# Performance work log

Measured on AMD Instinct MI355X. Metric: run time of the kernel, lower is better.

## Reference

```python
import jax, jax.numpy as jnp
import numpy as np

N = 200000   # active voxel sites
G = 80       # voxel grid extent per axis
K = 27       # 3x3x3 kernel offsets
CIN = 64
COUT = 128
EPS = 1e-5


def _build_rulebook(seed=0):
    """Submanifold 3x3x3 rulebook: for each offset k and output site i,
    in_idx[k,i] = index of neighbor site (or 0 if absent),
    out_idx[k,i] = i (or N = dummy row if neighbor absent)."""
    rng = np.random.default_rng(seed)
    lin = rng.choice(G ** 3, size=N, replace=False).astype(np.int64)
    lut = np.full(G ** 3, -1, dtype=np.int64)
    lut[lin] = np.arange(N)
    cx, cy, cz = lin // (G * G), (lin // G) % G, lin % G
    offs = [(dx, dy, dz) for dx in (-1, 0, 1) for dy in (-1, 0, 1) for dz in (-1, 0, 1)]
    in_idx = np.zeros((K, N), np.int32)
    out_idx = np.full((K, N), N, np.int32)
    ar = np.arange(N, dtype=np.int32)
    for k, (dx, dy, dz) in enumerate(offs):
        nx, ny, nz = cx + dx, cy + dy, cz + dz
        ok = (nx >= 0) & (nx < G) & (ny >= 0) & (ny < G) & (nz >= 0) & (nz < G)
        nb_lin = np.where(ok, nx * G * G + ny * G + nz, 0)
        j = lut[nb_lin]
        valid = ok & (j >= 0)
        in_idx[k] = np.where(valid, j, 0).astype(np.int32)
        out_idx[k] = np.where(valid, ar, N)
    return jnp.asarray(in_idx), jnp.asarray(out_idx)


def setup_inputs() -> dict:
    key = jax.random.key(0)
    ks = jax.random.split(key, 8)
    in_idx, out_idx = _build_rulebook(0)
    s1 = 1.0 / np.sqrt(CIN * K)
    s2 = 1.0 / np.sqrt(COUT * K)
    ss = 1.0 / np.sqrt(CIN)
    return {
        "feats": jax.random.normal(ks[0], (N, CIN), jnp.float32),
        "in_idx": in_idx,
        "out_idx": out_idx,
        "W1": jax.random.normal(ks[1], (K, CIN, COUT), jnp.float32) * s1,
        "g1": jnp.ones((COUT,), jnp.float32) + 0.1 * jax.random.normal(ks[2], (COUT,), jnp.float32),
        "b1": 0.1 * jax.random.normal(ks[3], (COUT,), jnp.float32),
        "W2": jax.random.normal(ks[4], (K, COUT, COUT), jnp.float32) * s2,
        "g2": jnp.ones((COUT,), jnp.float32) + 0.1 * jax.random.normal(ks[5], (COUT,), jnp.float32),
        "b2": 0.1 * jax.random.normal(ks[6], (COUT,), jnp.float32),
        "Wsc": jax.random.normal(ks[7], (CIN, COUT), jnp.float32) * ss,
        "gsc": jnp.ones((COUT,), jnp.float32),
        "bsc": jnp.zeros((COUT,), jnp.float32),
    }


def _spconv(feats, W, in_idx, out_idx):
    """Rulebook gather-GEMM-scatter sparse conv. feats [N,Cin], W [K,Cin,Cout]."""
    cout = W.shape[-1]
    out = jnp.zeros((N + 1, cout), feats.dtype)  # row N = dummy for padded pairs
    for k in range(K):  # fixed small structural loop over kernel offsets
        out = out.at[out_idx[k]].add(feats[in_idx[k]] @ W[k])
    return out[:N]


def _bn(x, gamma, beta):
    # training-mode BatchNorm over the site dimension (biased variance)
    m = jnp.mean(x, axis=0)
    v = jnp.var(x, axis=0)
    return (x - m) * jax.lax.rsqrt(v + EPS) * gamma + beta


def reference(feats, in_idx, out_idx, W1, g1, b1, W2, g2, b2, Wsc, gsc, bsc):
    h = jax.nn.relu(_bn(_spconv(feats, W1, in_idx, out_idx), g1, b1))
    h = _bn(_spconv(h, W2, in_idx, out_idx), g2, b2)
    sc = _bn(feats @ Wsc, gsc, bsc)  # 1x1 sparse conv == per-site linear
    return jax.nn.relu(h + sc)
```

## Files before the change

kernel.cpp:

```cpp
#include <hip/hip_runtime.h>

#define NS 200000
#define NK 27
#define NB2 1563
#define EPSV 1e-5f

typedef __bf16 bf16x8 __attribute__((ext_vector_type(8)));
typedef float f32x4 __attribute__((ext_vector_type(4)));
typedef unsigned short u16;
typedef u16 u16x8 __attribute__((ext_vector_type(8)));
typedef u16 u16x4 __attribute__((ext_vector_type(4)));
typedef unsigned u32;

__device__ __forceinline__ u16 f2bf(float f) {
  union { float f; unsigned u; } v; v.f = f;
  unsigned r = v.u + 0x7fffu + ((v.u >> 16) & 1u);
  return (u16)(r >> 16);
}
__device__ __forceinline__ float bf2f(u16 u) {
  union { unsigned u; float f; } v; v.u = ((unsigned)u) << 16;
  return v.f;
}

__global__ void k_prep_x(const float* __restrict__ feats, u16* __restrict__ Xbf,
                         float* __restrict__ stats) {
  long i = (long)blockIdx.x * 256 + threadIdx.x;
  if (i < 768) stats[i] = 0.f;
  const long total = (long)(NS + 1) * 64;
  if (i < total) {
    long row = i >> 6;
    Xbf[i] = (row < NS) ? f2bf(feats[i]) : (u16)0;
  }
}

__global__ void k_prep_gidx(const int* __restrict__ in_idx, const int* __restrict__ out_idx,
                            int* __restrict__ gidx) {
  long i = (long)blockIdx.x * 256 + threadIdx.x;
  if (i < (long)NK * NS) gidx[i] = (out_idx[i] != NS) ? in_idx[i] : NS;
}

__global__ void k_pack_w(const float* __restrict__ W1, const float* __restrict__ W2,
                         const float* __restrict__ Wsc, u16* __restrict__ Wp1,
                         u16* __restrict__ Wp2, u16* __restrict__ Wpsc) {
  int i = blockIdx.x * 256 + threadIdx.x;
  const int n1 = NK * 64 * 128, n2 = NK * 128 * 128, n3 = 64 * 128;
  const float* src; u16* dst; int f, S, C;
  if (i < n1)            { src = W1;  dst = Wp1;  f = i;            S = 2; C = 64; }
  else if (i < n1 + n2)  { src = W2;  dst = Wp2;  f = i - n1;       S = 4; C = 128; }
  else if (i < n1 + n2 + n3) { src = Wsc; dst = Wpsc; f = i - n1 - n2; S = 2; C = 64; }
  else return;
  int j = f & 7, q = (f >> 3) & 3, r = (f >> 5) & 15, cf = (f >> 9) & 7;
  int rest = f >> 12;
  int s = rest % S, k = rest / S;
  int kk = s * 32 + q * 8 + j;
  dst[f] = f2bf(src[(k * C + kk) * 128 + cf * 16 + r]);
}

template <int C, bool FUSE_SC>
__global__ __launch_bounds__(256, (C == 64) ? 3 : 2) void k_conv(
    const u16* __restrict__ X, const u16* __restrict__ Wp, const u16* __restrict__ Wpsc,
    const int* __restrict__ gidx,
    u16* __restrict__ Y, u16* __restrict__ SCb, float* __restrict__ partial) {
  constexpr int S = C / 32;
  constexpr int SLICE = C * 128;
  constexpr int NST = SLICE / 2048;
  constexpr int NG = 2 * S;
  constexpr int NW_STEADY = NG + 2 + NST + NG + 2;
  constexpr int PC = FUSE_SC ? 512 : 256;
  __shared__ alignas(16) u16 Wbuf[2 * SLICE];
  float* red = reinterpret_cast<float*>(&Wbuf[2 * SLICE - 2048]);

  const int t = threadIdx.x, w = t >> 6, l = t & 63;
  const int lr = l & 15, lh = l >> 4;
  const int rowbase = blockIdx.x * 128 + w * 32;
  const int laneoff = lr * 32 + lh * 8;

  int rr[2]; bool ok[2]; long rc[2];
  #pragma unroll
  for (int m = 0; m < 2; ++m) {
    rr[m] = rowbase + m * 16 + lr;
    ok[m] = rr[m] < NS;
    rc[m] = ok[m] ? rr[m] : 0;
  }

  auto stage = [&](int k, int bsel) {
    #pragma unroll
    for (int i = 0; i < NST; ++i) {
      const u16* g = Wp + (long)k * SLICE + (w * NST + i) * 512 + l * 8;
      u16* d = &Wbuf[bsel * SLICE + (w * NST + i) * 512];
      __builtin_amdgcn_global_load_lds(
          (const __attribute__((address_space(1))) u32*)g,
          (__attribute__((address_space(3))) u32*)d, 16, 0, 0);
    }
  };
  auto loadidx = [&](int k, int (&dst)[2]) {
    #pragma unroll
    for (int m = 0; m < 2; ++m) {
      int v = gidx[(long)k * NS + rc[m]];
      dst[m] = ok[m] ? v : NS;
    }
  };
  auto gather = [&](const int (&src)[2], bf16x8 (&a)[2][S]) {
    #pragma unroll
    for (int m = 0; m < 2; ++m) {
      const u16* rowp = X + (long)src[m] * C + lh * 8;
      #pragma unroll
      for (int s = 0; s < S; ++s)
        a[m][s] = *reinterpret_cast<const bf16x8*>(rowp + s * 32);
    }
  };
  auto compute = [&](int bsel, const bf16x8 (&a)[2][S], f32x4 (&ac)[2][8]) {
    #pragma unroll
    for (int s = 0; s < S; ++s)
      #pragma unroll
      for (int cf = 0; cf < 8; ++cf) {
        bf16x8 b = *reinterpret_cast<const bf16x8*>(&Wbuf[bsel * SLICE + (s * 8 + cf) * 512 + laneoff]);
        ac[0][cf] = __builtin_amdgcn_mfma_f32_16x16x32_bf16(a[0][s], b, ac[0][cf], 0, 0, 0);
        ac[1][cf] = __builtin_amdgcn_mfma_f32_16x16x32_bf16(a[1][s], b, ac[1][cf], 0, 0, 0);
      }
  };
  auto emit = [&](f32x4 (&ac)[2][8], u16* __restrict__ Yp, int poff) {
    #pragma unroll
    for (int m = 0; m < 2; ++m)
      #pragma unroll
      for (int cf = 0; cf < 8; ++cf) {
        int ch = cf * 16 + lr;
        #pragma unroll
        for (int r = 0; r < 4; ++r) {
          long row = rowbase + m * 16 + lh * 4 + r;
          if (row < NS) Yp[row * 128 + ch] = f2bf(ac[m][cf][r]);
        }
      }
    __syncthreads();
    #pragma unroll
    for (int cf = 0; cf < 8; ++cf) {
      float s = 0.f, q = 0.f;
      #pragma unroll
      for (int m = 0; m < 2; ++m)
        #pragma unroll
        for (int r = 0; r < 4; ++r) { float v = ac[m][cf][r]; s += v; q += v * v; }
      s += __shfl_xor(s, 16); s += __shfl_xor(s, 32);
      q += __shfl_xor(q, 16); q += __shfl_xor(q, 32);
      if (lh == 0) {
        red[w * 256 + cf * 16 + lr] = s;
        red[w * 256 + 128 + cf * 16 + lr] = q;
      }
    }
    __syncthreads();
    if (t < 256)
      partial[(long)blockIdx.x * PC + poff + t] =
          red[t] + red[256 + t] + red[512 + t] + red[768 + t];
    __syncthreads();
  };

  int sv0[2], sv1[2];
  bf16x8 av0[2][S], av1[2][S];
  loadidx(0, sv0);
  stage(0, 0);
  gather(sv0, av0);
  loadidx(1, sv1);

  if constexpr (FUSE_SC) {
    bf16x8 ai[2][S];
    #pragma unroll
    for (int m = 0; m < 2; ++m) {
      long srcr = ok[m] ? rr[m] : NS;
      #pragma unroll
      for (int s = 0; s < S; ++s)
        ai[m][s] = *reinterpret_cast<const bf16x8*>(X + srcr * C + lh * 8 + s * 32);
    }
    f32x4 asc[2][8];
    #pragma unroll
    for (int m = 0; m < 2; ++m)
      #pragma unroll
      for (int cf = 0; cf < 8; ++cf) asc[m][cf] = (f32x4){0.f, 0.f, 0.f, 0.f};
    #pragma unroll
    for (int s = 0; s < S; ++s)
      #pragma unroll
      for (int cf = 0; cf < 8; ++cf) {
        bf16x8 b = *reinterpret_cast<const bf16x8*>(Wpsc + (s * 8 + cf) * 512 + laneoff);
        asc[0][cf] = __builtin_amdgcn_mfma_f32_16x16x32_bf16(ai[0][s], b, asc[0][cf], 0, 0, 0);
        asc[1][cf] = __builtin_amdgcn_mfma_f32_16x16x32_bf16(ai[1][s], b, asc[1][cf], 0, 0, 0);
      }
    emit(asc, SCb, 256);
  }

  f32x4 acc[2][8];
  #pragma unroll
  for (int m = 0; m < 2; ++m)
    #pragma unroll
    for (int cf = 0; cf < 8; ++cf) acc[m][cf] = (f32x4){0.f, 0.f, 0.f, 0.f};

  #pragma unroll 1
  for (int k = 0; k < 24; k += 2) {
    stage(k + 1, 1);
    gather(sv1, av1);
    loadidx(k + 2, sv0);
    asm volatile("s_waitcnt vmcnt(%0)\n\ts_barrier" :: "i"(NW_STEADY) : "memory");
    compute(0, av0, acc);
    asm volatile("s_waitcnt lgkmcnt(0)\n\ts_barrier" ::: "memory");

    stage(k + 2, 0);
    gather(sv0, av0);
    loadidx(k + 3, sv1);
    asm volatile("s_waitcnt vmcnt(%0)\n\ts_barrier" :: "i"(NW_STEADY) : "memory");
    compute(1, av1, acc);
    asm volatile("s_waitcnt lgkmcnt(0)\n\ts_barrier" ::: "memory");
  }
  stage(25, 1);
  gather(sv1, av1);
  loadidx(26, sv0);
  asm volatile("s_waitcnt vmcnt(%0)\n\ts_barrier" :: "i"(NW_STEADY) : "memory");
  compute(0, av0, acc);
  asm volatile("s_waitcnt lgkmcnt(0)\n\ts_barrier" ::: "memory");

  stage(26, 0);
  gather(sv0, av0);
  asm volatile("s_waitcnt vmcnt(%0)\n\ts_barrier" :: "i"(NW_STEADY - 2) : "memory");
  compute(1, av1, acc);
  asm volatile("s_waitcnt lgkmcnt(0)\n\ts_barrier" ::: "memory");

  asm volatile("s_waitcnt vmcnt(%0)\n\ts_barrier" :: "i"(NG) : "memory");
  compute(0, av0, acc);

  emit(acc, Y, 0);
}

__global__ void k_red1(const float* __restrict__ part, float* __restrict__ tmp,
                       int pc, int nrows) {
  int c = blockIdx.x * 256 + threadIdx.x;
  float s = 0.f;
  for (int r = blockIdx.y; r < nrows; r += 32) s += part[(long)r * pc + c];
  tmp[(long)blockIdx.y * pc + c] = s;
}
__global__ void k_red2(const float* __restrict__ tmp, float* __restrict__ out, int pc) {
  int c = blockIdx.x * 256 + threadIdx.x;
  float s = 0.f;
  #pragma unroll
  for (int r = 0; r < 32; ++r) s += tmp[(long)r * pc + c];
  out[c] = s;
}

__global__ void k_bnrelu(const u16* __restrict__ Y1, const float* __restrict__ stats,
                         const float* __restrict__ g, const float* __restrict__ b,
                         u16* __restrict__ H) {
  long i8 = (long)blockIdx.x * 256 + threadIdx.x;
  const long tot = (long)(NS + 1) * 16;
  if (i8 >= tot) return;
  long row = i8 >> 4;
  u16x8 o;
  if (row < NS) {
    int ch0 = ((int)i8 & 15) * 8;
    u16x8 y = *reinterpret_cast<const u16x8*>(Y1 + i8 * 8);
    #pragma unroll
    for (int e = 0; e < 8; ++e) {
      int ch = ch0 + e;
      float m = stats[ch] * (1.f / NS);
      float var = stats[128 + ch] * (1.f / NS) - m * m;
      float a = g[ch] * rsqrtf(var + EPSV);
      float bb = b[ch] - m * a;
      float h = bf2f(y[e]) * a + bb;
      o[e] = f2bf(h > 0.f ? h : 0.f);
    }
  } else {
    #pragma unroll
    for (int e = 0; e < 8; ++e) o[e] = (u16)0;
  }
  *reinterpret_cast<u16x8*>(H + i8 * 8) = o;
}

__global__ void k_final(const u16* __restrict__ Y2, const u16* __restrict__ SCb,
                        const float* __restrict__ stats,
                        const float* __restrict__ g2, const float* __restrict__ b2,
                        const float* __restrict__ gsc, const float* __restrict__ bsc,
                        float* __restrict__ out) {
  long i4 = (long)blockIdx.x * 256 + threadIdx.x;
  if (i4 >= (long)NS * 32) return;
  int ch0 = ((int)i4 & 31) * 4;
  u16x4 y = *reinterpret_cast<const u16x4*>(Y2 + i4 * 4);
  u16x4 s = *reinterpret_cast<const u16x4*>(SCb + i4 * 4);
  f32x4 o;
  #pragma unroll
  for (int e = 0; e < 4; ++e) {
    int ch = ch0 + e;
    float m2 = stats[512 + ch] * (1.f / NS);
    float v2 = stats[640 + ch] * (1.f / NS) - m2 * m2;
    float a2 = g2[ch] * rsqrtf(v2 + EPSV);
    float msc = stats[256 + ch] * (1.f / NS);
    float vsc = stats[384 + ch] * (1.f / NS) - msc * msc;
    float asc = gsc[ch] * rsqrtf(vsc + EPSV);
    float val = bf2f(y[e]) * a2 + (b2[ch] - m2 * a2)
              + bf2f(s[e]) * asc + (bsc[ch] - msc * asc);
    o[e] = val > 0.f ? val : 0.f;
  }
  *reinterpret_cast<f32x4*>(out + i4 * 4) = o;
}

extern "C" void kernel_launch(void* const* d_in, const int* in_sizes, int n_in,
                              void* d_out, int out_size, void* d_ws, size_t ws_size,
                              hipStream_t stream) {
  const float* feats = (const float*)d_in[0];
  const int* in_idx  = (const int*)d_in[1];
  const int* out_idx = (const int*)d_in[2];
  const float* W1  = (const float*)d_in[3];
  const float* g1  = (const float*)d_in[4];
  const float* b1  = (const float*)d_in[5];
  const float* W2  = (const float*)d_in[6];
  const float* g2  = (const float*)d_in[7];
  const float* b2  = (const float*)d_in[8];
  const float* Wsc = (const float*)d_in[9];
  const float* gsc = (const float*)d_in[10];
  const float* bsc = (const float*)d_in[11];

  char* ws = (char*)d_ws;
  size_t off = 0;
  auto alloc = [&](size_t bytes) {
    void* p = ws + off; off += (bytes + 255) & ~(size_t)255; return p;
  };
  float* stats = (float*)alloc(768 * 4);
  float* rtmp  = (float*)alloc(32 * 512 * 4);
  u16* Xbf  = (u16*)alloc((size_t)(NS + 1) * 64 * 2);
  u16* SCbf = (u16*)alloc((size_t)NS * 128 * 2);
  u16* Hbf  = (u16*)alloc((size_t)(NS + 1) * 128 * 2);
  u16* Y2bf = (u16*)alloc((size_t)NS * 128 * 2);
  u16* Wp1  = (u16*)alloc((size_t)NK * 64 * 128 * 2);
  u16* Wp2  = (u16*)alloc((size_t)NK * 128 * 128 * 2);
  u16* Wpsc = (u16*)alloc((size_t)64 * 128 * 2);
  u16* Y1bf = (u16*)d_out;
  int* gidx = (int*)((char*)d_out + (size_t)NS * 128 * 2);
  float* part1 = (float*)Y2bf;
  float* part2 = (float*)Xbf;

  hipLaunchKernelGGL(k_prep_x, dim3(50001), dim3(256), 0, stream, feats, Xbf, stats);
  hipLaunchKernelGGL(k_prep_gidx, dim3((NK * NS + 255) / 256), dim3(256), 0, stream,
                     in_idx, out_idx, gidx);
  hipLaunchKernelGGL(k_pack_w, dim3(2624), dim3(256), 0, stream, W1, W2, Wsc, Wp1, Wp2, Wpsc);
  hipLaunchKernelGGL((k_conv<64, true>), dim3(NB2), dim3(256), 0, stream,
                     Xbf, Wp1, Wpsc, gidx, Y1bf, SCbf, part1);
  hipLaunchKernelGGL(k_red1, dim3(2, 32), dim3(256), 0, stream, part1, rtmp, 512, NB2);
  hipLaunchKernelGGL(k_red2, dim3(2), dim3(256), 0, stream, rtmp, stats, 512);
  hipLaunchKernelGGL(k_bnrelu, dim3(12501), dim3(256), 0, stream, Y1bf, stats, g1, b1, Hbf);
  hipLaunchKernelGGL((k_conv<128, false>), dim3(NB2), dim3(256), 0, stream,
                     Hbf, Wp2, nullptr, gidx, Y2bf, nullptr, part2);
  hipLaunchKernelGGL(k_red1, dim3(1, 32), dim3(256), 0, stream, part2, rtmp, 256, NB2);
  hipLaunchKernelGGL(k_red2, dim3(1), dim3(256), 0, stream, rtmp, stats + 512, 256);
  hipLaunchKernelGGL(k_final, dim3(25000), dim3(256), 0, stream,
                     Y2bf, SCbf, stats, g2, b2, gsc, bsc, (float*)d_out);
}
```

Before: 480.9 us.

## Double conv block size to 512 threads and repack weights for linear LDS reads

The sparse conv kernel now runs 8 waves per block covering 256 rows, so each staged weight slice in LDS is shared by twice as many rows and the grid is halved. The packed weight layout changes so each lane reads a contiguous 16-byte chunk (laneoff = l*8), which aims to cut LDS bank conflicts. The reduction buffer moves to its own shared array, one barrier is dropped, and MFMA sections are raised in wave priority with s_setprio. The larger block and separate reduction buffer raise LDS and register pressure per block, which may lower occupancy.

```diff
diff --git a/kernel.cpp b/kernel.cpp
--- a/kernel.cpp
+++ b/kernel.cpp
@@ -2,7 +2,7 @@
 
 #define NS 200000
 #define NK 27
-#define NB2 1563
+#define NBLK 782
 #define EPSV 1e-5f
 
 typedef __bf16 bf16x8 __attribute__((ext_vector_type(8)));
@@ -49,31 +49,31 @@
   else if (i < n1 + n2)  { src = W2;  dst = Wp2;  f = i - n1;       S = 4; C = 128; }
   else if (i < n1 + n2 + n3) { src = Wsc; dst = Wpsc; f = i - n1 - n2; S = 2; C = 64; }
   else return;
-  int j = f & 7, q = (f >> 3) & 3, r = (f >> 5) & 15, cf = (f >> 9) & 7;
+  int j = f & 7, l = (f >> 3) & 63, cf = (f >> 9) & 7;
   int rest = f >> 12;
   int s = rest % S, k = rest / S;
-  int kk = s * 32 + q * 8 + j;
-  dst[f] = f2bf(src[(k * C + kk) * 128 + cf * 16 + r]);
+  int kk = s * 32 + (l >> 4) * 8 + j;
+  dst[f] = f2bf(src[(k * C + kk) * 128 + cf * 16 + (l & 15)]);
 }
 
 template <int C, bool FUSE_SC>
-__global__ __launch_bounds__(256, (C == 64) ? 3 : 2) void k_conv(
+__global__ __launch_bounds__(512, 4) void k_conv(
     const u16* __restrict__ X, const u16* __restrict__ Wp, const u16* __restrict__ Wpsc,
     const int* __restrict__ gidx,
     u16* __restrict__ Y, u16* __restrict__ SCb, float* __restrict__ partial) {
   constexpr int S = C / 32;
   constexpr int SLICE = C * 128;
-  constexpr int NST = SLICE / 2048;
+  constexpr int NST = SLICE / 4096;
   constexpr int NG = 2 * S;
   constexpr int NW_STEADY = NG + 2 + NST + NG + 2;
   constexpr int PC = FUSE_SC ? 512 : 256;
   __shared__ alignas(16) u16 Wbuf[2 * SLICE];
-  float* red = reinterpret_cast<float*>(&Wbuf[2 * SLICE - 2048]);
+  __shared__ float red[2048];
 
   const int t = threadIdx.x, w = t >> 6, l = t & 63;
   const int lr = l & 15, lh = l >> 4;
-  const int rowbase = blockIdx.x * 128 + w * 32;
-  const int laneoff = lr * 32 + lh * 8;
+  const int rowbase = blockIdx.x * 256 + w * 32;
+  const int laneoff = l * 8;
 
   int rr[2]; bool ok[2]; long rc[2];
   #pragma unroll
@@ -110,6 +110,7 @@
     }
   };
   auto compute = [&](int bsel, const bf16x8 (&a)[2][S], f32x4 (&ac)[2][8]) {
+    __builtin_amdgcn_s_setprio(1);
     #pragma unroll
     for (int s = 0; s < S; ++s)
       #pragma unroll
@@ -118,6 +119,7 @@
         ac[0][cf] = __builtin_amdgcn_mfma_f32_16x16x32_bf16(a[0][s], b, ac[0][cf], 0, 0, 0);
         ac[1][cf] = __builtin_amdgcn_mfma_f32_16x16x32_bf16(a[1][s], b, ac[1][cf], 0, 0, 0);
       }
+    __builtin_amdgcn_s_setprio(0);
   };
   auto emit = [&](f32x4 (&ac)[2][8], u16* __restrict__ Yp, int poff) {
     #pragma unroll
@@ -131,7 +133,6 @@
           if (row < NS) Yp[row * 128 + ch] = f2bf(ac[m][cf][r]);
         }
       }
-    __syncthreads();
     #pragma unroll
     for (int cf = 0; cf < 8; ++cf) {
       float s = 0.f, q = 0.f;
@@ -147,9 +148,12 @@
       }
     }
     __syncthreads();
-    if (t < 256)
-      partial[(long)blockIdx.x * PC + poff + t] =
-          red[t] + red[256 + t] + red[512 + t] + red[768 + t];
+    if (t < 256) {
+      float sum = 0.f;
+      #pragma unroll
+      for (int wi = 0; wi < 8; ++wi) sum += red[wi * 256 + t];
+      partial[(long)blockIdx.x * PC + poff + t] = sum;
+    }
     __syncthreads();
   };
 
@@ -335,14 +339,14 @@
   hipLaunchKernelGGL(k_prep_gidx, dim3((NK * NS + 255) / 256), dim3(256), 0, stream,
                      in_idx, out_idx, gidx);
   hipLaunchKernelGGL(k_pack_w, dim3(2624), dim3(256), 0, stream, W1, W2, Wsc, Wp1, Wp2, Wpsc);
-  hipLaunchKernelGGL((k_conv<64, true>), dim3(NB2), dim3(256), 0, stream,
+  hipLaunchKernelGGL((k_conv<64, true>), dim3(NBLK), dim3(512), 0, stream,
                      Xbf, Wp1, Wpsc, gidx, Y1bf, SCbf, part1);
-  hipLaunchKernelGGL(k_red1, dim3(2, 32), dim3(256), 0, stream, part1, rtmp, 512, NB2);
+  hipLaunchKernelGGL(k_red1, dim3(2, 32), dim3(256), 0, stream, part1, rtmp, 512, NBLK);
   hipLaunchKernelGGL(k_red2, dim3(2), dim3(256), 0, stream, rtmp, stats, 512);
   hipLaunchKernelGGL(k_bnrelu, dim3(12501), dim3(256), 0, stream, Y1bf, stats, g1, b1, Hbf);
-  hipLaunchKernelGGL((k_conv<128, false>), dim3(NB2), dim3(256), 0, stream,
+  hipLaunchKernelGGL((k_conv<128, false>), dim3(NBLK), dim3(512), 0, stream,
                      Hbf, Wp2, nullptr, gidx, Y2bf, nullptr, part2);
-  hipLaunchKernelGGL(k_red1, dim3(1, 32), dim3(256), 0, stream, part2, rtmp, 256, NB2);
+  hipLaunchKernelGGL(k_red1, dim3(1, 32), dim3(256), 0, stream, part2, rtmp, 256, NBLK);
   hipLaunchKernelGGL(k_red2, dim3(1), dim3(256), 0, stream, rtmp, stats + 512, 256);
   hipLaunchKernelGGL(k_final, dim3(25000), dim3(256), 0, stream,
                      Y2bf, SCbf, stats, g2, b2, gsc, bsc, (float*)d_out);
```

Result: slower. 707.3 us (+47.1%).

## Skip gathers for absent neighbors, restructure conv pipeline waits, add MFMA priority

Applied to the files above, without the earlier changes.

The conv main loop is restructured. Each gather is issued after a barrier that waits only on staged weights and index loads, and the epilogue is folded into the loop by clamping the last index load. Gathers for missing neighbors are now skipped and zero-filled, so the padded dummy row and its write in prep and bnrelu are removed. Compute sections raise wave priority with s_setprio, and the weight packing and LDS read offset change to a linear per-lane layout. The aim is less wasted memory traffic on sparse neighbors and better overlap, at the cost of gathers now sitting closer to the compute that uses them.

```diff
diff --git a/kernel.cpp b/kernel.cpp
--- a/kernel.cpp
+++ b/kernel.cpp
@@ -2,7 +2,7 @@
 
 #define NS 200000
 #define NK 27
-#define NB2 1563
+#define NB 1563
 #define EPSV 1e-5f
 
 typedef __bf16 bf16x8 __attribute__((ext_vector_type(8)));
@@ -26,11 +26,8 @@
                          float* __restrict__ stats) {
   long i = (long)blockIdx.x * 256 + threadIdx.x;
   if (i < 768) stats[i] = 0.f;
-  const long total = (long)(NS + 1) * 64;
-  if (i < total) {
-    long row = i >> 6;
-    Xbf[i] = (row < NS) ? f2bf(feats[i]) : (u16)0;
-  }
+  const long total = (long)NS * 64;
+  if (i < total) Xbf[i] = f2bf(feats[i]);
 }
 
 __global__ void k_prep_gidx(const int* __restrict__ in_idx, const int* __restrict__ out_idx,
@@ -49,11 +46,11 @@
   else if (i < n1 + n2)  { src = W2;  dst = Wp2;  f = i - n1;       S = 4; C = 128; }
   else if (i < n1 + n2 + n3) { src = Wsc; dst = Wpsc; f = i - n1 - n2; S = 2; C = 64; }
   else return;
-  int j = f & 7, q = (f >> 3) & 3, r = (f >> 5) & 15, cf = (f >> 9) & 7;
+  int j = f & 7, l = (f >> 3) & 63, cf = (f >> 9) & 7;
   int rest = f >> 12;
   int s = rest % S, k = rest / S;
-  int kk = s * 32 + q * 8 + j;
-  dst[f] = f2bf(src[(k * C + kk) * 128 + cf * 16 + r]);
+  int kk = s * 32 + (l >> 4) * 8 + j;
+  dst[f] = f2bf(src[(k * C + kk) * 128 + cf * 16 + (l & 15)]);
 }
 
 template <int C, bool FUSE_SC>
@@ -63,17 +60,16 @@
     u16* __restrict__ Y, u16* __restrict__ SCb, float* __restrict__ partial) {
   constexpr int S = C / 32;
   constexpr int SLICE = C * 128;
-  constexpr int NST = SLICE / 2048;
-  constexpr int NG = 2 * S;
-  constexpr int NW_STEADY = NG + 2 + NST + NG + 2;
+  constexpr int NST = C / 16;
+  constexpr int WAITN = NST + 4;
   constexpr int PC = FUSE_SC ? 512 : 256;
   __shared__ alignas(16) u16 Wbuf[2 * SLICE];
-  float* red = reinterpret_cast<float*>(&Wbuf[2 * SLICE - 2048]);
+  float* red = reinterpret_cast<float*>(Wbuf);
 
   const int t = threadIdx.x, w = t >> 6, l = t & 63;
   const int lr = l & 15, lh = l >> 4;
   const int rowbase = blockIdx.x * 128 + w * 32;
-  const int laneoff = lr * 32 + lh * 8;
+  const int laneoff = l * 8;
 
   int rr[2]; bool ok[2]; long rc[2];
   #pragma unroll
@@ -83,11 +79,11 @@
     rc[m] = ok[m] ? rr[m] : 0;
   }
 
-  auto stage = [&](int k, int bsel) {
+  auto stage = [&](int k, int p) {
     #pragma unroll
     for (int i = 0; i < NST; ++i) {
       const u16* g = Wp + (long)k * SLICE + (w * NST + i) * 512 + l * 8;
-      u16* d = &Wbuf[bsel * SLICE + (w * NST + i) * 512];
+      u16* d = &Wbuf[p * SLICE + (w * NST + i) * 512];
       __builtin_amdgcn_global_load_lds(
           (const __attribute__((address_space(1))) u32*)g,
           (__attribute__((address_space(3))) u32*)d, 16, 0, 0);
@@ -103,21 +99,28 @@
   auto gather = [&](const int (&src)[2], bf16x8 (&a)[2][S]) {
     #pragma unroll
     for (int m = 0; m < 2; ++m) {
-      const u16* rowp = X + (long)src[m] * C + lh * 8;
-      #pragma unroll
-      for (int s = 0; s < S; ++s)
-        a[m][s] = *reinterpret_cast<const bf16x8*>(rowp + s * 32);
-    }
-  };
-  auto compute = [&](int bsel, const bf16x8 (&a)[2][S], f32x4 (&ac)[2][8]) {
+      #pragma unroll
+      for (int s = 0; s < S; ++s) a[m][s] = bf16x8{};
+      if (src[m] != NS) {
+        const u16* rowp = X + (long)src[m] * C + lh * 8;
+        #pragma unroll
+        for (int s = 0; s < S; ++s)
+          a[m][s] = *reinterpret_cast<const bf16x8*>(rowp + s * 32);
+      }
+    }
+  };
+  auto compute = [&](int p, const bf16x8 (&a)[2][S], f32x4 (&ac)[2][8]) {
+    __builtin_amdgcn_s_setprio(1);
     #pragma unroll
     for (int s = 0; s < S; ++s)
       #pragma unroll
       for (int cf = 0; cf < 8; ++cf) {
-        bf16x8 b = *reinterpret_cast<const bf16x8*>(&Wbuf[bsel * SLICE + (s * 8 + cf) * 512 + laneoff]);
+        bf16x8 b = *reinterpret_cast<const bf16x8*>(
+            &Wbuf[p * SLICE + (s * 8 + cf) * 512 + laneoff]);
         ac[0][cf] = __builtin_amdgcn_mfma_f32_16x16x32_bf16(a[0][s], b, ac[0][cf], 0, 0, 0);
         ac[1][cf] = __builtin_amdgcn_mfma_f32_16x16x32_bf16(a[1][s], b, ac[1][cf], 0, 0, 0);
       }
+    __builtin_amdgcn_s_setprio(0);
   };
   auto emit = [&](f32x4 (&ac)[2][8], u16* __restrict__ Yp, int poff) {
     #pragma unroll
@@ -153,74 +156,64 @@
     __syncthreads();
   };
 
+  if constexpr (FUSE_SC) {
+    bf16x8 ai[2][2];
+    #pragma unroll
+    for (int m = 0; m < 2; ++m) {
+      #pragma unroll
+      for (int s = 0; s < 2; ++s) ai[m][s] = bf16x8{};
+      if (ok[m]) {
+        #pragma unroll
+        for (int s = 0; s < 2; ++s)
+          ai[m][s] = *reinterpret_cast<const bf16x8*>(X + (long)rr[m] * 64 + lh * 8 + s * 32);
+      }
+    }
+    f32x4 asc[2][8];
+    #pragma unroll
+    for (int m = 0; m < 2; ++m)
+      #pragma unroll
+      for (int cf = 0; cf < 8; ++cf) asc[m][cf] = (f32x4){0.f, 0.f, 0.f, 0.f};
+    #pragma unroll
+    for (int s = 0; s < 2; ++s)
+      #pragma unroll
+      for (int cf = 0; cf < 8; ++cf) {
+        bf16x8 b = *reinterpret_cast<const bf16x8*>(Wpsc + (s * 8 + cf) * 512 + laneoff);
+        asc[0][cf] = __builtin_amdgcn_mfma_f32_16x16x32_bf16(ai[0][s], b, asc[0][cf], 0, 0, 0);
+        asc[1][cf] = __builtin_amdgcn_mfma_f32_16x16x32_bf16(ai[1][s], b, asc[1][cf], 0, 0, 0);
+      }
+    emit(asc, SCb, 256);
+  }
+
+  f32x4 acc[2][8];
+  #pragma unroll
+  for (int m = 0; m < 2; ++m)
+    #pragma unroll
+    for (int cf = 0; cf < 8; ++cf) acc[m][cf] = (f32x4){0.f, 0.f, 0.f, 0.f};
+
   int sv0[2], sv1[2];
   bf16x8 av0[2][S], av1[2][S];
+
   loadidx(0, sv0);
   stage(0, 0);
   gather(sv0, av0);
   loadidx(1, sv1);
 
-  if constexpr (FUSE_SC) {
-    bf16x8 ai[2][S];
-    #pragma unroll
-    for (int m = 0; m < 2; ++m) {
-      long srcr = ok[m] ? rr[m] : NS;
-      #pragma unroll
-      for (int s = 0; s < S; ++s)
-        ai[m][s] = *reinterpret_cast<const bf16x8*>(X + srcr * C + lh * 8 + s * 32);
-    }
-    f32x4 asc[2][8];
-    #pragma unroll
-    for (int m = 0; m < 2; ++m)
-      #pragma unroll
-      for (int cf = 0; cf < 8; ++cf) asc[m][cf] = (f32x4){0.f, 0.f, 0.f, 0.f};
-    #pragma unroll
-    for (int s = 0; s < S; ++s)
-      #pragma unroll
-      for (int cf = 0; cf < 8; ++cf) {
-        bf16x8 b = *reinterpret_cast<const bf16x8*>(Wpsc + (s * 8 + cf) * 512 + laneoff);
-        asc[0][cf] = __builtin_amdgcn_mfma_f32_16x16x32_bf16(ai[0][s], b, asc[0][cf], 0, 0, 0);
-        asc[1][cf] = __builtin_amdgcn_mfma_f32_16x16x32_bf16(ai[1][s], b, asc[1][cf], 0, 0, 0);
-      }
-    emit(asc, SCb, 256);
-  }
-
-  f32x4 acc[2][8];
-  #pragma unroll
-  for (int m = 0; m < 2; ++m)
-    #pragma unroll
-    for (int cf = 0; cf < 8; ++cf) acc[m][cf] = (f32x4){0.f, 0.f, 0.f, 0.f};
-
   #pragma unroll 1
-  for (int k = 0; k < 24; k += 2) {
+  for (int k = 0; k < NK - 1; k += 2) {
     stage(k + 1, 1);
+    loadidx(k + 2, sv0);
+    asm volatile("s_waitcnt vmcnt(%0)\n\ts_barrier" :: "i"(WAITN) : "memory");
     gather(sv1, av1);
-    loadidx(k + 2, sv0);
-    asm volatile("s_waitcnt vmcnt(%0)\n\ts_barrier" :: "i"(NW_STEADY) : "memory");
     compute(0, av0, acc);
     asm volatile("s_waitcnt lgkmcnt(0)\n\ts_barrier" ::: "memory");
-
     stage(k + 2, 0);
+    { int kn = k + 3 < NK ? k + 3 : NK - 1; loadidx(kn, sv1); }
+    asm volatile("s_waitcnt vmcnt(%0)\n\ts_barrier" :: "i"(WAITN) : "memory");
     gather(sv0, av0);
-    loadidx(k + 3, sv1);
-    asm volatile("s_waitcnt vmcnt(%0)\n\ts_barrier" :: "i"(NW_STEADY) : "memory");
     compute(1, av1, acc);
     asm volatile("s_waitcnt lgkmcnt(0)\n\ts_barrier" ::: "memory");
   }
-  stage(25, 1);
-  gather(sv1, av1);
-  loadidx(26, sv0);
-  asm volatile("s_waitcnt vmcnt(%0)\n\ts_barrier" :: "i"(NW_STEADY) : "memory");
-  compute(0, av0, acc);
-  asm volatile("s_waitcnt lgkmcnt(0)\n\ts_barrier" ::: "memory");
-
-  stage(26, 0);
-  gather(sv0, av0);
-  asm volatile("s_waitcnt vmcnt(%0)\n\ts_barrier" :: "i"(NW_STEADY - 2) : "memory");
-  compute(1, av1, acc);
-  asm volatile("s_waitcnt lgkmcnt(0)\n\ts_barrier" ::: "memory");
-
-  asm volatile("s_waitcnt vmcnt(%0)\n\ts_barrier" :: "i"(NG) : "memory");
+  asm volatile("s_waitcnt vmcnt(0)\n\ts_barrier" ::: "memory");
   compute(0, av0, acc);
 
   emit(acc, Y, 0);
@@ -245,26 +238,20 @@
                          const float* __restrict__ g, const float* __restrict__ b,
                          u16* __restrict__ H) {
   long i8 = (long)blockIdx.x * 256 + threadIdx.x;
-  const long tot = (long)(NS + 1) * 16;
+  const long tot = (long)NS * 16;
   if (i8 >= tot) return;
-  long row = i8 >> 4;
+  int ch0 = ((int)i8 & 15) * 8;
+  u16x8 y = *reinterpret_cast<const u16x8*>(Y1 + i8 * 8);
   u16x8 o;
-  if (row < NS) {
-    int ch0 = ((int)i8 & 15) * 8;
-    u16x8 y = *reinterpret_cast<const u16x8*>(Y1 + i8 * 8);
-    #pragma unroll
-    for (int e = 0; e < 8; ++e) {
-      int ch = ch0 + e;
-      float m = stats[ch] * (1.f / NS);
-      float var = stats[128 + ch] * (1.f / NS) - m * m;
-      float a = g[ch] * rsqrtf(var + EPSV);
-      float bb = b[ch] - m * a;
-      float h = bf2f(y[e]) * a + bb;
-      o[e] = f2bf(h > 0.f ? h : 0.f);
-    }
-  } else {
-    #pragma unroll
-    for (int e = 0; e < 8; ++e) o[e] = (u16)0;
+  #pragma unroll
+  for (int e = 0; e < 8; ++e) {
+    int ch = ch0 + e;
+    float m = stats[ch] * (1.f / NS);
+    float var = stats[128 + ch] * (1.f / NS) - m * m;
+    float a = g[ch] * rsqrtf(var + EPSV);
+    float bb = b[ch] - m * a;
+    float h = bf2f(y[e]) * a + bb;
+    o[e] = f2bf(h > 0.f ? h : 0.f);
   }
   *reinterpret_cast<u16x8*>(H + i8 * 8) = o;
 }
@@ -319,9 +306,9 @@
   };
   float* stats = (float*)alloc(768 * 4);
   float* rtmp  = (float*)alloc(32 * 512 * 4);
-  u16* Xbf  = (u16*)alloc((size_t)(NS + 1) * 64 * 2);
+  u16* Xbf  = (u16*)alloc((size_t)NS * 64 * 2);
   u16* SCbf = (u16*)alloc((size_t)NS * 128 * 2);
-  u16* Hbf  = (u16*)alloc((size_t)(NS + 1) * 128 * 2);
+  u16* Hbf  = (u16*)alloc((size_t)NS * 128 * 2);
   u16* Y2bf = (u16*)alloc((size_t)NS * 128 * 2);
   u16* Wp1  = (u16*)alloc((size_t)NK * 64 * 128 * 2);
   u16* Wp2  = (u16*)alloc((size_t)NK * 128 * 128 * 2);
@@ -331,18 +318,18 @@
   float* part1 = (float*)Y2bf;
   float* part2 = (float*)Xbf;
 
-  hipLaunchKernelGGL(k_prep_x, dim3(50001), dim3(256), 0, stream, feats, Xbf, stats);
+  hipLaunchKernelGGL(k_prep_x, dim3(50000), dim3(256), 0, stream, feats, Xbf, stats);
   hipLaunchKernelGGL(k_prep_gidx, dim3((NK * NS + 255) / 256), dim3(256), 0, stream,
                      in_idx, out_idx, gidx);
   hipLaunchKernelGGL(k_pack_w, dim3(2624), dim3(256), 0, stream, W1, W2, Wsc, Wp1, Wp2, Wpsc);
-  hipLaunchKernelGGL((k_conv<64, true>), dim3(NB2), dim3(256), 0, stream,
+  hipLaunchKernelGGL((k_conv<64, true>), dim3(NB), dim3(256), 0, stream,
                      Xbf, Wp1, Wpsc, gidx, Y1bf, SCbf, part1);
-  hipLaunchKernelGGL(k_red1, dim3(2, 32), dim3(256), 0, stream, part1, rtmp, 512, NB2);
+  hipLaunchKernelGGL(k_red1, dim3(2, 32), dim3(256), 0, stream, part1, rtmp, 512, NB);
   hipLaunchKernelGGL(k_red2, dim3(2), dim3(256), 0, stream, rtmp, stats, 512);
-  hipLaunchKernelGGL(k_bnrelu, dim3(12501), dim3(256), 0, stream, Y1bf, stats, g1, b1, Hbf);
-  hipLaunchKernelGGL((k_conv<128, false>), dim3(NB2), dim3(256), 0, stream,
+  hipLaunchKernelGGL(k_bnrelu, dim3(12500), dim3(256), 0, stream, Y1bf, stats, g1, b1, Hbf);
+  hipLaunchKernelGGL((k_conv<128, false>), dim3(NB), dim3(256), 0, stream,
                      Hbf, Wp2, nullptr, gidx, Y2bf, nullptr, part2);
-  hipLaunchKernelGGL(k_red1, dim3(1, 32), dim3(256), 0, stream, part2, rtmp, 256, NB2);
+  hipLaunchKernelGGL(k_red1, dim3(1, 32), dim3(256), 0, stream, part2, rtmp, 256, NB);
   hipLaunchKernelGGL(k_red2, dim3(1), dim3(256), 0, stream, rtmp, stats + 512, 256);
   hipLaunchKernelGGL(k_final, dim3(25000), dim3(256), 0, stream,
                      Y2bf, SCbf, stats, g2, b2, gsc, bsc, (float*)d_out);
```

New measurement: 497.1 us. 1.03x slower.
